# Performance work log

Measured on AMD Instinct MI355X. Metric: run time of the kernel, lower is better.

## Reference

```python
import jax, jax.numpy as jnp
import numpy as np
import math

B, S, D, H = 1, 2048, 2048, 16
DH = D // H  # 128
HALF = DH // 2  # 64


def setup_inputs() -> dict:
    key = jax.random.key(0)
    ks = jax.random.split(key, 6)
    x = jax.random.normal(ks[0], (B, S, D), dtype=jnp.float32)
    # rotary frequencies: freqs_cis = exp(i * t * theta), theta_j = 10000^{-2j/DH}
    inv_freq = 1.0 / (10000.0 ** (np.arange(0, DH, 2, dtype=np.float32) / DH))  # [HALF]
    t = np.arange(S, dtype=np.float32)
    angles = np.outer(t, inv_freq)  # [S, HALF]
    freqs_cos = jnp.asarray(np.cos(angles), dtype=jnp.float32)
    freqs_sin = jnp.asarray(np.sin(angles), dtype=jnp.float32)
    # additive causal mask [1,1,S,S]
    mask = jnp.triu(jnp.full((S, S), -1e9, dtype=jnp.float32), k=1)[None, None]
    scale = 0.02
    wq = jax.random.normal(ks[1], (D, D), dtype=jnp.float32) * scale
    wk = jax.random.normal(ks[2], (D, D), dtype=jnp.float32) * scale
    wv = jax.random.normal(ks[3], (D, D), dtype=jnp.float32) * scale
    wo = jax.random.normal(ks[4], (D, D), dtype=jnp.float32) * scale
    return {"x": x, "freqs_cos": freqs_cos, "freqs_sin": freqs_sin, "mask": mask,
            "wq": wq, "wk": wk, "wv": wv, "wo": wo, "start_pos": 0}


def _apply_rope(t, cos, sin):
    # t: [B,S,H,DH]; cos/sin: [S,HALF] broadcast as [1,S,1,HALF]
    tr = t.reshape(*t.shape[:-1], HALF, 2)
    even, odd = tr[..., 0], tr[..., 1]
    c = cos[None, :, None, :]
    s = sin[None, :, None, :]
    out_even = even * c - odd * s
    out_odd = even * s + odd * c
    return jnp.stack([out_even, out_odd], axis=-1).reshape(t.shape)


def reference(x, freqs_cos, freqs_sin, mask, wq, wk, wv, wo, start_pos):
    bsz, seqlen, _ = x.shape
    q = (x @ wq.T).reshape(bsz, seqlen, H, DH)
    k = (x @ wk.T).reshape(bsz, seqlen, H, DH)
    v = (x @ wv.T).reshape(bsz, seqlen, H, DH)
    q = _apply_rope(q, freqs_cos, freqs_sin)
    k = _apply_rope(k, freqs_cos, freqs_sin)
    q = q.transpose(0, 2, 1, 3)  # [B,H,S,DH]
    k = k.transpose(0, 2, 1, 3)
    v = v.transpose(0, 2, 1, 3)
    scores = jnp.einsum('bhqd,bhkd->bhqk', q, k) / math.sqrt(DH) + mask
    probs = jax.nn.softmax(scores, axis=-1)
    out = jnp.einsum('bhqk,bhkd->bhqd', probs, v)  # [B,H,S,DH]
    # faithful to original: transpose(2,3) then view(bsz, seqlen, dim)
    out = out.transpose(0, 1, 3, 2).reshape(bsz, seqlen, D)
    return out @ wo.T
```

## Files before the change

### kernel.cpp

```cpp
#include <hip/hip_runtime.h>

typedef unsigned short u16;
typedef unsigned int   u32;
typedef short  short8   __attribute__((ext_vector_type(8)));
typedef float  floatx4  __attribute__((ext_vector_type(4)));
typedef u16    ushortx2 __attribute__((ext_vector_type(2)));
typedef u16    ushortx4 __attribute__((ext_vector_type(4)));

__device__ __forceinline__ float bf2f(u16 u) {
  union { u32 i; float f; } v; v.i = ((u32)u) << 16; return v.f;
}
__device__ __forceinline__ u16 f2bf(float x) {
  union { float f; u32 i; } v; v.f = x;
  u32 r = v.i + 0x7FFFu + ((v.i >> 16) & 1u);
  return (u16)(r >> 16);
}

#if __has_builtin(__builtin_amdgcn_exp2f)
#define EXP2F(x) __builtin_amdgcn_exp2f(x)
#else
#define EXP2F(x) __exp2f(x)
#endif

#define GLOAD_LDS16(gptr, lptr)                                                   \
  __builtin_amdgcn_global_load_lds(                                               \
      (const __attribute__((address_space(1))) void*)(gptr),                      \
      (__attribute__((address_space(3))) void*)(lptr), 16, 0, 0)

#define WAITV(n) asm volatile("s_waitcnt vmcnt(" #n ")" ::: "memory")
#define WAITL    asm volatile("s_waitcnt lgkmcnt(0)" ::: "memory")
#define BAR      __builtin_amdgcn_s_barrier()

__global__ __launch_bounds__(256) void cvt_all(
    const floatx4* __restrict__ x,  const floatx4* __restrict__ wq,
    const floatx4* __restrict__ wk, const floatx4* __restrict__ wv,
    const floatx4* __restrict__ wo,
    ushortx4* __restrict__ xb, ushortx4* __restrict__ wqkv,
    ushortx4* __restrict__ wob) {
  int i = blockIdx.x * 256 + threadIdx.x;
  const floatx4* in; ushortx4* out;
  switch (blockIdx.y) {
    case 0:  in = x;  out = xb; break;
    case 1:  in = wq; out = wqkv; break;
    case 2:  in = wk; out = wqkv + (size_t)1048576; break;
    case 3:  in = wv; out = wqkv + (size_t)2097152; break;
    default: in = wo; out = wob; break;
  }
  floatx4 v = in[i];
  ushortx4 o;
  o.x = f2bf(v.x); o.y = f2bf(v.y); o.z = f2bf(v.z); o.w = f2bf(v.w);
  out[i] = o;
}

__global__ __launch_bounds__(512, 2) void gemm256_bt(
    const u16* __restrict__ A, const u16* __restrict__ B, u16* __restrict__ C,
    int N, int K, int lda, int ldb, int ldc) {
  const int cpx = gridDim.x >> 3;
  const int wg = ((int)blockIdx.x & 7) * cpx + ((int)blockIdx.x >> 3);
  const int ntn = N >> 8;
  const int m0 = (wg / ntn) << 8;
  const int n0 = (wg % ntn) << 8;

  __shared__ __align__(16) u16 As[2][256][64];
  __shared__ __align__(16) u16 Bs[2][256][64];

  const int t = threadIdx.x;
  const int lane = t & 63;
  const int wave = t >> 6;
  const int wr = wave >> 2;
  const int wc = wave & 3;
  const int quad = lane >> 4;
  const int mrow = lane & 15;
  const int sw = mrow & 7;

  const int srow = lane >> 3;
  const int gso  = ((lane & 7) ^ srow) << 3;

  const u16* gA = A + (size_t)(m0 + (wave << 3) + srow) * lda + gso;
  const u16* gB = B + (size_t)(n0 + (wave << 3) + srow) * ldb + gso;

  floatx4 acc[8][4] = {};
  short8 afr[4][2], bfr[4][2];

  const int NT = K >> 6;

#define ST_A(nb, h, kt)                                                        \
  do {                                                                         \
    GLOAD_LDS16(gA + (size_t)((h) * 128) * lda + ((kt) << 6),                  \
                &As[nb][(h) * 128 + (wave << 3)][0]);                          \
    GLOAD_LDS16(gA + (size_t)((h) * 128 + 64) * lda + ((kt) << 6),             \
                &As[nb][(h) * 128 + 64 + (wave << 3)][0]);                     \
  } while (0)
#define ST_B(nb, h, kt)                                                        \
  do {                                                                         \
    GLOAD_LDS16(gB + (size_t)((h) * 128) * ldb + ((kt) << 6),                  \
                &Bs[nb][(h) * 128 + (wave << 3)][0]);                          \
    GLOAD_LDS16(gB + (size_t)((h) * 128 + 64) * ldb + ((kt) << 6),             \
                &Bs[nb][(h) * 128 + 64 + (wave << 3)][0]);                     \
  } while (0)

#define LDA4(bf, base_row)                                                     \
  do {                                                                         \
    _Pragma("unroll") for (int i_ = 0; i_ < 4; i_++)                           \
      _Pragma("unroll") for (int kk_ = 0; kk_ < 2; kk_++)                      \
        afr[i_][kk_] = *(const short8*)&As[bf][(base_row) + (i_ << 4) + mrow]  \
                            [(((kk_ << 2) | quad) ^ sw) << 3];                 \
  } while (0)
#define LDB2(bf, jlo, base_row)                                                \
  do {                                                                         \
    _Pragma("unroll") for (int j_ = 0; j_ < 2; j_++)                           \
      _Pragma("unroll") for (int kk_ = 0; kk_ < 2; kk_++)                      \
        bfr[(jlo) + j_][kk_] =                                                 \
            *(const short8*)&Bs[bf][(base_row) + (j_ << 4) + mrow]             \
                [(((kk_ << 2) | quad) ^ sw) << 3];                             \
  } while (0)
#define MMQ(ilo, jlo)                                                          \
  do {                                                                         \
    __builtin_amdgcn_s_setprio(1);                                             \
    _Pragma("unroll") for (int kk_ = 0; kk_ < 2; kk_++)                        \
      _Pragma("unroll") for (int i_ = 0; i_ < 4; i_++)                         \
        _Pragma("unroll") for (int j_ = 0; j_ < 2; j_++)                       \
          acc[(ilo) + i_][(jlo) + j_] =                                        \
              __builtin_amdgcn_mfma_f32_16x16x32_bf16(                         \
                  afr[i_][kk_], bfr[(jlo) + j_][kk_],                          \
                  acc[(ilo) + i_][(jlo) + j_], 0, 0, 0);                       \
    __builtin_amdgcn_s_setprio(0);                                             \
  } while (0)

  ST_A(0, 0, 0); ST_B(0, 0, 0); ST_B(0, 1, 0); ST_A(0, 1, 0);
  WAITV(4);
  BAR;

  for (int kt = 0; kt < NT - 1; kt++) {
    const int bf = kt & 1, nb = bf ^ 1;
    LDA4(bf, (wr << 6));
    LDB2(bf, 0, (wc << 5));
    ST_A(nb, 0, kt + 1);
    WAITV(4);
    BAR;
    MMQ(0, 0);
    LDB2(bf, 2, 128 + (wc << 5));
    ST_B(nb, 0, kt + 1);
    WAITV(4);
    BAR;
    MMQ(0, 2);
    LDA4(bf, 128 + (wr << 6));
    ST_B(nb, 1, kt + 1);
    BAR;
    MMQ(4, 2);
    ST_A(nb, 1, kt + 1);
    WAITL;
    WAITV(4);
    BAR;
    MMQ(4, 0);
  }
  {
    const int bf = (NT - 1) & 1;
    LDA4(bf, (wr << 6));
    LDB2(bf, 0, (wc << 5));
    WAITV(2);
    BAR;
    MMQ(0, 0);
    LDB2(bf, 2, 128 + (wc << 5));
    WAITV(0);
    BAR;
    MMQ(0, 2);
    LDA4(bf, 128 + (wr << 6));
    WAITL;
    BAR;
    MMQ(4, 2);
    MMQ(4, 0);
  }

#pragma unroll
  for (int i = 0; i < 8; i++) {
    int row0 = m0 + ((i >= 4) ? 128 : 0) + (wr << 6) + ((i & 3) << 4) + (quad << 2);
#pragma unroll
    for (int j = 0; j < 4; j++) {
      int col = n0 + ((j >= 2) ? 128 : 0) + (wc << 5) + ((j & 1) << 4) + mrow;
#pragma unroll
      for (int r = 0; r < 4; r++)
        C[(size_t)(row0 + r) * ldc + col] = f2bf(acc[i][j][r]);
    }
  }
#undef ST_A
#undef ST_B
#undef LDA4
#undef LDB2
#undef MMQ
}

__global__ __launch_bounds__(256) void gemm_bt(
    const u16* __restrict__ A, const u16* __restrict__ B, void* __restrict__ Cv,
    int M, int N, int K, int lda, int ldb, int ldc,
    long batchA, long batchB, long batchC, int outBF16) {
  const int m0 = blockIdx.y << 7;
  const int n0 = blockIdx.x << 7;

  A += (long)blockIdx.z * batchA;
  B += (long)blockIdx.z * batchB;
  const long cbase = (long)blockIdx.z * batchC;

  __shared__ __align__(16) u16 As[128][64];
  __shared__ __align__(16) u16 Bs[128][64];

  const int t = threadIdx.x;
  const int lane = t & 63;
  const int wave = t >> 6;
  const int wm = (wave >> 1) << 6;
  const int wn = (wave & 1) << 6;
  const int quad = lane >> 4;
  const int mrow = lane & 15;
  const int sw8 = mrow & 7;

  floatx4 acc[4][4] = {};

  const int srow = lane >> 3;
  const int gseg = (((lane & 7) ^ srow) << 3);
  const u16* gA = A + (long)(m0 + (wave << 5) + srow) * lda + gseg;
  const u16* gB = B + (long)(n0 + (wave << 5) + srow) * ldb + gseg;

  for (int k0 = 0; k0 < K; k0 += 64) {
    __syncthreads();
#pragma unroll
    for (int ii = 0; ii < 4; ii++) {
      GLOAD_LDS16(gA + k0 + (size_t)(ii << 3) * lda, &As[(wave << 5) + (ii << 3)][0]);
      GLOAD_LDS16(gB + k0 + (size_t)(ii << 3) * ldb, &Bs[(wave << 5) + (ii << 3)][0]);
    }
    __syncthreads();

#pragma unroll
    for (int kh = 0; kh < 2; kh++) {
      const int sidx = ((kh << 2) | quad) ^ sw8;
      short8 af[4], bfr[4];
#pragma unroll
      for (int i = 0; i < 4; i++)
        af[i] = *(const short8*)&As[wm + (i << 4) + mrow][sidx << 3];
#pragma unroll
      for (int j = 0; j < 4; j++)
        bfr[j] = *(const short8*)&Bs[wn + (j << 4) + mrow][sidx << 3];
#pragma unroll
      for (int i = 0; i < 4; i++)
#pragma unroll
        for (int j = 0; j < 4; j++)
          acc[i][j] = __builtin_amdgcn_mfma_f32_16x16x32_bf16(af[i], bfr[j], acc[i][j], 0, 0, 0);
    }
  }

#pragma unroll
  for (int i = 0; i < 4; i++) {
    int row0 = m0 + wm + (i << 4) + (quad << 2);
#pragma unroll
    for (int j = 0; j < 4; j++) {
      int col = n0 + wn + (j << 4) + mrow;
#pragma unroll
      for (int r = 0; r < 4; r++) {
        long idx = cbase + (long)(row0 + r) * ldc + col;
        float val = acc[i][j][r];
        if (outBF16) ((u16*)Cv)[idx] = f2bf(val);
        else         ((float*)Cv)[idx] = val;
      }
    }
  }
}

__global__ __launch_bounds__(256) void transpose_v(const u16* __restrict__ src,
                                                   u16* __restrict__ dst) {
  __shared__ u16 tile[64][68];
  const int d0 = blockIdx.x << 6;
  const int s0 = blockIdx.y << 6;
  const int tx = (threadIdx.x & 15) << 2;
  const int ty = threadIdx.x >> 4;
#pragma unroll
  for (int rr = 0; rr < 64; rr += 16) {
    ushortx4 v = *(const ushortx4*)(src + (size_t)(s0 + ty + rr) * 6144 + d0 + tx);
    *(ushortx4*)&tile[ty + rr][tx] = v;
  }
  __syncthreads();
#pragma unroll
  for (int rr = 0; rr < 64; rr += 16) {
    int r = ty + rr;
    ushortx4 o;
    o.x = tile[tx + 0][r]; o.y = tile[tx + 1][r];
    o.z = tile[tx + 2][r]; o.w = tile[tx + 3][r];
    *(ushortx4*)(dst + (size_t)(d0 + r) * 2048 + s0 + tx) = o;
  }
}

__global__ __launch_bounds__(256) void rope_qk(u16* __restrict__ qkv,
                                               const float* __restrict__ cs,
                                               const float* __restrict__ sn) {
  int idx = blockIdx.x * 256 + threadIdx.x;
  int p = idx & 63;
  int h = (idx >> 6) & 15;
  int s = idx >> 10;
  float c  = cs[(s << 6) | p];
  float si = sn[(s << 6) | p];
  float scale = blockIdx.y ? 1.0f : 0.12751743f;
  size_t off = (size_t)s * 6144 + (blockIdx.y ? 2048 : 0) + (h << 7) + (p << 1);
  ushortx2 eo = *(ushortx2*)(qkv + off);
  float e = bf2f(eo.x), o = bf2f(eo.y);
  ushortx2 r;
  r.x = f2bf((e * c - o * si) * scale);
  r.y = f2bf((e * si + o * c) * scale);
  *(ushortx2*)(qkv + off) = r;
}

__global__ __launch_bounds__(256, 2) void flash_attn(
    const u16* __restrict__ QKVp, const u16* __restrict__ VTp,
    u16* __restrict__ ATp) {
  const int r0id = (int)blockIdx.x + ((int)blockIdx.y << 5);
  const int h    = r0id & 15;
  const int qsub = 31 - (r0id >> 4);
  const int q0 = qsub << 6;
  const int ktmax = qsub >> 1;

  __shared__ __align__(16) u16 Ks[128][128];
  __shared__ __align__(16) u16 Vs[128][128];
  __shared__ __align__(16) u16 Ps[64][128];

  const int t = threadIdx.x;
  const int lane = t & 63;
  const int wave = t >> 6;
  const int quad = lane >> 4;
  const int mrow = lane & 15;
  const int sw   = mrow & 7;
  const int wmS = (wave & 1) << 5;
  const int wnS = (wave >> 1) << 6;
  const int wmV = (wave >> 1) << 6;
  const int wnP = (wave & 1) << 5;

  const int r4  = lane >> 4;
  const int seg = lane & 15;
  const int c0 = ((seg ^ r4) << 3);
  const int c4 = ((seg ^ (r4 + 4)) << 3);

  const u16* qbase = QKVp + (size_t)q0 * 6144 + (h << 7);
  const u16* kbase = QKVp + 2048 + (h << 7);
  const u16* vbase = VTp + (size_t)(h << 7) * 2048;

  short8 aq[2][4];
#pragma unroll
  for (int i = 0; i < 2; i++)
#pragma unroll
    for (int kk = 0; kk < 4; kk++)
      aq[i][kk] = *(const short8*)(qbase + (size_t)(wmS + (i << 4) + mrow) * 6144 +
                                   (kk << 5) + (quad << 3));

  const short8 ones = {0x3F80, 0x3F80, 0x3F80, 0x3F80,
                       0x3F80, 0x3F80, 0x3F80, 0x3F80};

  floatx4 Oa[4][2] = {};
  floatx4 Oa1[2] = {};

  const float C2 = 23.083120654223414f;

  for (int kt = 0; kt <= ktmax; kt++) {
    __syncthreads();
    {
      int rr0 = wave << 5;
#pragma unroll
      for (int ii = 0; ii < 8; ii++) {
        int rr = rr0 + (ii << 2);
        GLOAD_LDS16(kbase + (size_t)((kt << 7) + rr + r4) * 6144 + ((ii & 1) ? c4 : c0),
                    &Ks[rr][0]);
        GLOAD_LDS16(vbase + (size_t)(rr + r4) * 2048 + (kt << 7) + ((ii & 1) ? c4 : c0),
                    &Vs[rr][0]);
      }
    }
    __syncthreads();

    floatx4 sa[2][4] = {};
#pragma unroll
    for (int kk = 0; kk < 4; kk++) {
      short8 bk[4];
#pragma unroll
      for (int j = 0; j < 4; j++)
        bk[j] = *(const short8*)&Ks[wnS + (j << 4) + mrow][(((kk << 2) | quad) ^ sw) << 3];
#pragma unroll
      for (int i = 0; i < 2; i++)
#pragma unroll
        for (int j = 0; j < 4; j++)
          sa[i][j] = __builtin_amdgcn_mfma_f32_16x16x32_bf16(aq[i][kk], bk[j], sa[i][j], 0, 0, 0);
    }
    if (kt == ktmax) {
#pragma unroll
      for (int i = 0; i < 2; i++)
#pragma unroll
        for (int j = 0; j < 4; j++)
#pragma unroll
          for (int r = 0; r < 4; r++) {
            int ql = q0 + wmS + (i << 4) + (quad << 2) + r;
            int sl = (kt << 7) + wnS + (j << 4) + mrow;
            if (sl > ql) sa[i][j][r] = -1e30f;
          }
    }
#pragma unroll
    for (int i = 0; i < 2; i++)
#pragma unroll
      for (int j = 0; j < 4; j++)
#pragma unroll
        for (int r = 0; r < 4; r++) {
          int row = wmS + (i << 4) + (quad << 2) + r;
          int col = wnS + (j << 4) + mrow;
          Ps[row][((((col >> 3) ^ (row & 7)) << 3) | (col & 7))] =
              f2bf(EXP2F(sa[i][j][r] - C2));
        }
    __syncthreads();

#pragma unroll
    for (int kk = 0; kk < 4; kk++) {
      short8 av[4], bp[2];
#pragma unroll
      for (int i = 0; i < 4; i++)
        av[i] = *(const short8*)&Vs[wmV + (i << 4) + mrow][(((kk << 2) | quad) ^ sw) << 3];
#pragma unroll
      for (int j = 0; j < 2; j++)
        bp[j] = *(const short8*)&Ps[wnP + (j << 4) + mrow][(((kk << 2) | quad) ^ sw) << 3];
#pragma unroll
      for (int i = 0; i < 4; i++)
#pragma unroll
        for (int j = 0; j < 2; j++)
          Oa[i][j] = __builtin_amdgcn_mfma_f32_16x16x32_bf16(av[i], bp[j], Oa[i][j], 0, 0, 0);
#pragma unroll
      for (int j = 0; j < 2; j++)
        Oa1[j] = __builtin_amdgcn_mfma_f32_16x16x32_bf16(ones, bp[j], Oa1[j], 0, 0, 0);
    }
  }

  float linv[2];
#pragma unroll
  for (int j = 0; j < 2; j++) linv[j] = 1.f / Oa1[j][0];
#pragma unroll
  for (int i = 0; i < 4; i++) {
    int drow = (h << 7) + wmV + (i << 4) + (quad << 2);
#pragma unroll
    for (int j = 0; j < 2; j++) {
      int col = q0 + wnP + (j << 4) + mrow;
#pragma unroll
      for (int r = 0; r < 4; r++)
        ATp[(size_t)(drow + r) * 2048 + col] = f2bf(Oa[i][j][r] * linv[j]);
    }
  }
}

__global__ __launch_bounds__(256) void reduce2(const floatx4* __restrict__ a,
                                               const floatx4* __restrict__ b,
                                               floatx4* __restrict__ o) {
  int i = blockIdx.x * 256 + threadIdx.x;
  o[i] = a[i] + b[i];
}

extern "C" void kernel_launch(void* const* d_in, const int* in_sizes, int n_in,
                              void* d_out, int out_size, void* d_ws, size_t ws_size,
                              hipStream_t stream) {
  const float* x  = (const float*)d_in[0];
  const float* fc = (const float*)d_in[1];
  const float* fs = (const float*)d_in[2];
  const float* wq = (const float*)d_in[4];
  const float* wk = (const float*)d_in[5];
  const float* wv = (const float*)d_in[6];
  const float* wo = (const float*)d_in[7];
  float* out = (float*)d_out;

  char* ws = (char*)d_ws;
  const size_t MB = 1024 * 1024;
  u16*   XB   = (u16*)(ws + 0 * MB);
  u16*   WQKV = (u16*)(ws + 8 * MB);
  u16*   WOb  = (u16*)(ws + 32 * MB);
  u16*   QKV  = (u16*)(ws + 40 * MB);
  u16*   VT   = (u16*)(ws + 64 * MB);
  u16*   AT   = (u16*)(ws + 72 * MB);
  float* PART = (float*)(ws + 80 * MB);

  int use_split = (ws_size >= 113 * MB);

  dim3 blk(256);
  cvt_all<<<dim3(4096, 5), blk, 0, stream>>>(
      (const floatx4*)x, (const floatx4*)wq, (const floatx4*)wk,
      (const floatx4*)wv, (const floatx4*)wo,
      (ushortx4*)XB, (ushortx4*)WQKV, (ushortx4*)WOb);

  gemm256_bt<<<dim3(192), dim3(512), 0, stream>>>(XB, WQKV, QKV,
                                                  6144, 2048, 2048, 2048, 6144);

  transpose_v<<<dim3(32, 32), blk, 0, stream>>>(QKV + 4096, VT);
  rope_qk<<<dim3(8192, 2), blk, 0, stream>>>(QKV, fc, fs);

  flash_attn<<<dim3(32, 16), blk, 0, stream>>>(QKV, VT, AT);

  if (use_split) {
    gemm_bt<<<dim3(16, 16, 2), blk, 0, stream>>>(AT, WOb, PART, 2048, 2048, 1024,
                                                 2048, 2048, 2048,
                                                 1024, 1024, (long)2048 * 2048, 0);
    reduce2<<<4096, blk, 0, stream>>>((const floatx4*)PART,
                                      (const floatx4*)(PART + (size_t)2048 * 2048),
                                      (floatx4*)out);
  } else {
    gemm_bt<<<dim3(16, 16, 1), blk, 0, stream>>>(AT, WOb, out, 2048, 2048, 2048,
                                                 2048, 2048, 2048, 0, 0, 0, 0);
  }
}
```

Before: 289.1 us.

## Retile QKV GEMM to 256x192 tiles so the grid fills 256 CUs

Changes the QKV projection GEMM tile from 256x256 to 256x192, raising the workgroup count from 192 to 256. The aim is to match the 256 compute units on MI355X and remove idle CUs in a single wave. The B staging, LDS fragment loads, MFMA schedule and wait counts are rebuilt around three 64-row B chunks. In exchange each tile has a lower compute-to-load ratio and the pipeline waits had to be retuned, which could expose memory latency.

```diff
diff --git a/kernel.cpp b/kernel.cpp
--- a/kernel.cpp
+++ b/kernel.cpp
@@ -57,12 +57,12 @@
     int N, int K, int lda, int ldb, int ldc) {
   const int cpx = gridDim.x >> 3;
   const int wg = ((int)blockIdx.x & 7) * cpx + ((int)blockIdx.x >> 3);
-  const int ntn = N >> 8;
+  const int ntn = N / 192;
   const int m0 = (wg / ntn) << 8;
-  const int n0 = (wg % ntn) << 8;
+  const int n0 = (wg % ntn) * 192;
 
   __shared__ __align__(16) u16 As[2][256][64];
-  __shared__ __align__(16) u16 Bs[2][256][64];
+  __shared__ __align__(16) u16 Bs[2][192][64];
 
   const int t = threadIdx.x;
   const int lane = t & 63;
@@ -79,8 +79,8 @@
   const u16* gA = A + (size_t)(m0 + (wave << 3) + srow) * lda + gso;
   const u16* gB = B + (size_t)(n0 + (wave << 3) + srow) * ldb + gso;
 
-  floatx4 acc[8][4] = {};
-  short8 afr[4][2], bfr[4][2];
+  floatx4 acc[8][3] = {};
+  short8 afr[4][2], bfr[3][2];
 
   const int NT = K >> 6;
 
@@ -91,12 +91,10 @@
     GLOAD_LDS16(gA + (size_t)((h) * 128 + 64) * lda + ((kt) << 6),             \
                 &As[nb][(h) * 128 + 64 + (wave << 3)][0]);                     \
   } while (0)
-#define ST_B(nb, h, kt)                                                        \
+#define ST_B1(nb, c, kt)                                                       \
   do {                                                                         \
-    GLOAD_LDS16(gB + (size_t)((h) * 128) * ldb + ((kt) << 6),                  \
-                &Bs[nb][(h) * 128 + (wave << 3)][0]);                          \
-    GLOAD_LDS16(gB + (size_t)((h) * 128 + 64) * ldb + ((kt) << 6),             \
-                &Bs[nb][(h) * 128 + 64 + (wave << 3)][0]);                     \
+    GLOAD_LDS16(gB + (size_t)((c) * 64) * ldb + ((kt) << 6),                   \
+                &Bs[nb][(c) * 64 + (wave << 3)][0]);                           \
   } while (0)
 
 #define LDA4(bf, base_row)                                                     \
@@ -106,88 +104,93 @@
         afr[i_][kk_] = *(const short8*)&As[bf][(base_row) + (i_ << 4) + mrow]  \
                             [(((kk_ << 2) | quad) ^ sw) << 3];                 \
   } while (0)
-#define LDB2(bf, jlo, base_row)                                                \
+#define LDB1(bf, j)                                                            \
   do {                                                                         \
-    _Pragma("unroll") for (int j_ = 0; j_ < 2; j_++)                           \
-      _Pragma("unroll") for (int kk_ = 0; kk_ < 2; kk_++)                      \
-        bfr[(jlo) + j_][kk_] =                                                 \
-            *(const short8*)&Bs[bf][(base_row) + (j_ << 4) + mrow]             \
-                [(((kk_ << 2) | quad) ^ sw) << 3];                             \
+    _Pragma("unroll") for (int kk_ = 0; kk_ < 2; kk_++)                        \
+      bfr[j][kk_] = *(const short8*)&Bs[bf][(j) * 64 + (wc << 4) + mrow]       \
+          [(((kk_ << 2) | quad) ^ sw) << 3];                                   \
   } while (0)
-#define MMQ(ilo, jlo)                                                          \
+#define MMQ8(ilo, j)                                                           \
   do {                                                                         \
     __builtin_amdgcn_s_setprio(1);                                             \
     _Pragma("unroll") for (int kk_ = 0; kk_ < 2; kk_++)                        \
       _Pragma("unroll") for (int i_ = 0; i_ < 4; i_++)                         \
-        _Pragma("unroll") for (int j_ = 0; j_ < 2; j_++)                       \
-          acc[(ilo) + i_][(jlo) + j_] =                                        \
-              __builtin_amdgcn_mfma_f32_16x16x32_bf16(                         \
-                  afr[i_][kk_], bfr[(jlo) + j_][kk_],                          \
-                  acc[(ilo) + i_][(jlo) + j_], 0, 0, 0);                       \
+        acc[(ilo) + i_][j] = __builtin_amdgcn_mfma_f32_16x16x32_bf16(          \
+            afr[i_][kk_], bfr[j][kk_], acc[(ilo) + i_][j], 0, 0, 0);           \
     __builtin_amdgcn_s_setprio(0);                                             \
   } while (0)
 
-  ST_A(0, 0, 0); ST_B(0, 0, 0); ST_B(0, 1, 0); ST_A(0, 1, 0);
+  ST_A(0, 0, 0); ST_B1(0, 0, 0); ST_B1(0, 1, 0); ST_B1(0, 2, 0); ST_A(0, 1, 0);
   WAITV(4);
   BAR;
 
   for (int kt = 0; kt < NT - 1; kt++) {
     const int bf = kt & 1, nb = bf ^ 1;
     LDA4(bf, (wr << 6));
-    LDB2(bf, 0, (wc << 5));
+    LDB1(bf, 0);
     ST_A(nb, 0, kt + 1);
+    WAITV(5);
+    BAR;
+    MMQ8(0, 0);
+    LDB1(bf, 1);
+    ST_B1(nb, 0, kt + 1);
+    WAITV(5);
+    BAR;
+    MMQ8(0, 1);
+    LDB1(bf, 2);
+    ST_B1(nb, 1, kt + 1);
     WAITV(4);
     BAR;
-    MMQ(0, 0);
-    LDB2(bf, 2, 128 + (wc << 5));
-    ST_B(nb, 0, kt + 1);
-    WAITV(4);
-    BAR;
-    MMQ(0, 2);
+    MMQ8(0, 2);
     LDA4(bf, 128 + (wr << 6));
-    ST_B(nb, 1, kt + 1);
-    BAR;
-    MMQ(4, 2);
+    ST_B1(nb, 2, kt + 1);
+    BAR;
+    MMQ8(4, 0);
     ST_A(nb, 1, kt + 1);
     WAITL;
     WAITV(4);
     BAR;
-    MMQ(4, 0);
+    MMQ8(4, 1);
+    MMQ8(4, 2);
   }
   {
     const int bf = (NT - 1) & 1;
     LDA4(bf, (wr << 6));
-    LDB2(bf, 0, (wc << 5));
+    LDB1(bf, 0);
+    WAITV(3);
+    BAR;
+    MMQ8(0, 0);
+    LDB1(bf, 1);
     WAITV(2);
     BAR;
-    MMQ(0, 0);
-    LDB2(bf, 2, 128 + (wc << 5));
+    MMQ8(0, 1);
+    LDB1(bf, 2);
     WAITV(0);
     BAR;
-    MMQ(0, 2);
+    MMQ8(0, 2);
     LDA4(bf, 128 + (wr << 6));
-    WAITL;
-    BAR;
-    MMQ(4, 2);
-    MMQ(4, 0);
+    BAR;
+    MMQ8(4, 0);
+    MMQ8(4, 1);
+    MMQ8(4, 2);
   }
 
 #pragma unroll
   for (int i = 0; i < 8; i++) {
     int row0 = m0 + ((i >= 4) ? 128 : 0) + (wr << 6) + ((i & 3) << 4) + (quad << 2);
 #pragma unroll
-    for (int j = 0; j < 4; j++) {
-      int col = n0 + ((j >= 2) ? 128 : 0) + (wc << 5) + ((j & 1) << 4) + mrow;
+    for (int j = 0; j < 3; j++) {
+      int col = n0 + j * 64 + (wc << 4) + mrow;
 #pragma unroll
       for (int r = 0; r < 4; r++)
         C[(size_t)(row0 + r) * ldc + col] = f2bf(acc[i][j][r]);
     }
   }
 #undef ST_A
-#undef ST_B
+#undef ST_B1
 #undef LDA4
-#undef LDB2
-#undef MMQ
+#undef LDB1
+#undef MMQ8
 }
 
 __global__ __launch_bounds__(256) void gemm_bt(
@@ -481,7 +484,7 @@
       (const floatx4*)wv, (const floatx4*)wo,
       (ushortx4*)XB, (ushortx4*)WQKV, (ushortx4*)WOb);
 
-  gemm256_bt<<<dim3(192), dim3(512), 0, stream>>>(XB, WQKV, QKV,
+  gemm256_bt<<<dim3(256), dim3(512), 0, stream>>>(XB, WQKV, QKV,
                                                   6144, 2048, 2048, 2048, 6144);
 
   transpose_v<<<dim3(32, 32), blk, 0, stream>>>(QKV + 4096, VT);
```

Result: no change. 283.7 us (-1.9%).
